# Kernel optimization log

Hardware: AMD Instinct MI355X
Metric: run time of the kernel (lower is better)

## Reference

```python
import jax, jax.numpy as jnp
import numpy as np

B, T, D = 2, 2048, 2048
H = 8
DK = 256   # head_qk_dim
DV = 512   # head_v_dim
C = 64     # retention chunk size
EPS = 1e-5
ROPE_BASE = 10000.0


def _rotary(x):
    # x: [B, T, H, DK], non-interleaved (rotate-half) rotary over full head dim
    half = DK // 2
    inv_freq = 1.0 / (ROPE_BASE ** (jnp.arange(0, DK, 2, dtype=jnp.float32) / DK))
    freqs = jnp.arange(T, dtype=jnp.float32)[:, None] * inv_freq[None, :]  # [T, half]
    cos = jnp.cos(freqs)[None, :, None, :].astype(x.dtype)
    sin = jnp.sin(freqs)[None, :, None, :].astype(x.dtype)
    x1, x2 = x[..., :half], x[..., half:]
    return jnp.concatenate([x1 * cos - x2 * sin, x2 * cos + x1 * sin], axis=-1)


def setup_inputs() -> dict:
    key = jax.random.key(0)
    ks = jax.random.split(key, 6)
    s = 2.0 ** (-2.5) * (2.0 / 2048.0) ** 0.5  # xavier_uniform-ish scale, gain 2^-2.5
    return {
        "hidden_states": jax.random.normal(ks[0], (B, T, D), jnp.float32),
        "Wq": jax.random.normal(ks[1], (H * DK, D), jnp.float32) * s,
        "Wk": jax.random.normal(ks[2], (H * DK, D), jnp.float32) * s,
        "Wv": jax.random.normal(ks[3], (H * DV, D), jnp.float32) * s,
        "Wg": jax.random.normal(ks[4], (H * DV, D), jnp.float32) * s,
        "Wo": jax.random.normal(ks[5], (D, H * DV), jnp.float32) * s,
        "g_norm_weight": jnp.ones((DV,), jnp.float32),
    }


def reference(hidden_states, Wq, Wk, Wv, Wg, Wo, g_norm_weight):
    x = hidden_states  # [B, T, D]
    q = (x @ Wq.T).reshape(B, T, H, DK)
    k = (x @ Wk.T).reshape(B, T, H, DK)
    q = _rotary(q)
    k = _rotary(k)
    q = q.transpose(0, 2, 1, 3) * (DK ** -0.5)        # [B, H, T, DK]
    k = k.transpose(0, 2, 1, 3)                       # [B, H, T, DK]
    v = (x @ Wv.T).reshape(B, T, H, DV).transpose(0, 2, 1, 3)  # [B, H, T, DV]

    # RetNet multi-scale per-head decay
    logb = jnp.log(1.0 - 2.0 ** (-5.0 - jnp.arange(H, dtype=jnp.float32)))  # [H]
    i = jnp.arange(C, dtype=jnp.float32)
    # intra-chunk decay mask b^{i-j} for i>=j: [H, C, C]
    Dmask = jnp.where(i[:, None] >= i[None, :],
                      jnp.exp(logb[:, None, None] * (i[:, None] - i[None, :])), 0.0)
    q_dec = jnp.exp(logb[:, None] * (i + 1.0))        # [H, C]  decay applied to q vs carried state
    k_dec = jnp.exp(logb[:, None] * (C - 1.0 - i))    # [H, C]  decay applied to k for state update
    chunk_dec = jnp.exp(logb * C)                     # [H]

    N = T // C
    qc = q.reshape(B, H, N, C, DK).transpose(2, 0, 1, 3, 4)  # [N, B, H, C, DK]
    kc = k.reshape(B, H, N, C, DK).transpose(2, 0, 1, 3, 4)
    vc = v.reshape(B, H, N, C, DV).transpose(2, 0, 1, 3, 4)

    def body(S, inp):
        qi, ki, vi = inp  # [B,H,C,DK], [B,H,C,DK], [B,H,C,DV]
        inter = jnp.einsum('bhcd,bhdv->bhcv', qi * q_dec[None, :, :, None], S)
        scores = jnp.einsum('bhcd,bhmd->bhcm', qi, ki) * Dmask[None]
        o = inter + jnp.einsum('bhcm,bhmv->bhcv', scores, vi)
        S_new = S * chunk_dec[None, :, None, None] + \
                jnp.einsum('bhcd,bhcv->bhdv', ki * k_dec[None, :, :, None], vi)
        return S_new, o

    S0 = jnp.zeros((B, H, DK, DV), x.dtype)
    _, oc = jax.lax.scan(body, S0, (qc, kc, vc))  # oc: [N, B, H, C, DV]
    o = oc.transpose(1, 2, 0, 3, 4).reshape(B, H, T, DV).transpose(0, 2, 1, 3)  # [B, T, H, DV]

    g = (x @ Wg.T).reshape(B, T, H, DV)
    # fused RMSNorm + swish gate (per head_v_dim)
    o_n = o * jax.lax.rsqrt(jnp.mean(o * o, axis=-1, keepdims=True) + EPS) * g_norm_weight
    o = o_n * (g * jax.nn.sigmoid(g))
    return o.reshape(B, T, H * DV) @ Wo.T  # [B, T, D]
```

## Files before the change

kernel.cpp:

```cpp
#include <hip/hip_runtime.h>


typedef unsigned short u16;
typedef unsigned int u32;
typedef short bf16x8 __attribute__((ext_vector_type(8)));
typedef short s16x4 __attribute__((ext_vector_type(4)));
typedef float f32x4 __attribute__((ext_vector_type(4)));
typedef u32 u32x2 __attribute__((ext_vector_type(2)));

typedef __attribute__((address_space(3))) u32 lds_u32;
typedef __attribute__((address_space(1))) const u32 gbl_u32;

__device__ __forceinline__ float bf2f(u16 u) {
    union { u32 i; float f; } x; x.i = ((u32)u) << 16; return x.f;
}
__device__ __forceinline__ u16 f2bf(float f) {
    union { float f; u32 i; } x; x.f = f;
    u32 u = x.i;
    u += 0x7fffu + ((u >> 16) & 1u);
    return (u16)(u >> 16);
}
__device__ __forceinline__ f32x4 mfma16(bf16x8 a, bf16x8 b, f32x4 c) {
    return __builtin_amdgcn_mfma_f32_16x16x32_bf16(a, b, c, 0, 0, 0);
}
__device__ __forceinline__ void gload16(const u16* g, u16* lds) {
    __builtin_amdgcn_global_load_lds((gbl_u32*)(unsigned long long)g,
                                     (lds_u32*)(u32)(unsigned long long)lds, 16, 0, 0);
}

__global__ __launch_bounds__(256)
void cvt_bf16(const float* __restrict__ src, u16* __restrict__ dst)
{
    size_t i = ((size_t)blockIdx.x * 256 + threadIdx.x) * 8;
    f32x4 a = *(const f32x4*)(src + i);
    f32x4 b = *(const f32x4*)(src + i + 4);
    bf16x8 r;
#pragma unroll
    for (int j = 0; j < 4; j++) { r[j] = (short)f2bf(a[j]); r[j + 4] = (short)f2bf(b[j]); }
    *(bf16x8*)(dst + i) = r;
}

__global__ __launch_bounds__(512, 2)
void gemm256(const u16* __restrict__ A, const u16* __restrict__ Bm,
             u16* __restrict__ C, int N, int K)
{
    __shared__ __align__(16) u16 As[2][2][256 * 32];
    __shared__ __align__(16) u16 Bs[2][2][256 * 32];
    const int tid = threadIdx.x;
    const int lane = tid & 63, wave = tid >> 6;
    const int quad = lane >> 4, l16 = lane & 15;
    const int wm = wave >> 2, wn = wave & 3;
    const int tn = blockIdx.x, tm = blockIdx.y;
    const int NTm1 = K / 64 - 1;
    const u16* Abase = A + (size_t)tm * 256 * K;
    const u16* Bbase = Bm + (size_t)tn * 256 * K;
    const int gr = tid >> 2;
    const int gc = (tid & 3) * 8;
    const int wv64 = wave * 64;

    f32x4 acc[8][4];
#pragma unroll
    for (int i = 0; i < 8; i++)
#pragma unroll
        for (int j = 0; j < 4; j++) acc[i][j] = (f32x4){0.f, 0.f, 0.f, 0.f};

    bf16x8 bq[8];
    bf16x8 af[4];

#define STAGE(arr, bf, kc, Gb, kt) do {                                         \
    int kt_ = (kt); kt_ = (kt_ > NTm1) ? NTm1 : kt_;                            \
    const u16* s_ = (Gb) + (size_t)gr * K + (size_t)kt_ * 64 + (kc) * 32 + gc;  \
    gload16(s_,                 &arr[bf][kc][wv64 * 8]);                        \
    gload16(s_ + (size_t)128 * K, &arr[bf][kc][(512 + wv64) * 8]);              \
} while (0)

#define LDA(bf, kc, mg) do {                                                    \
    _Pragma("unroll")                                                           \
    for (int j = 0; j < 4; j++)                                                 \
        af[j] = *(const bf16x8*)&As[bf][kc][(wm * 128 + (mg) * 64 + j * 16 + l16) * 32 + quad * 8]; \
} while (0)

#define LDB(bf) do {                                                            \
    _Pragma("unroll")                                                           \
    for (int kc_ = 0; kc_ < 2; kc_++)                                           \
        _Pragma("unroll")                                                       \
        for (int n_ = 0; n_ < 4; n_++)                                          \
            bq[kc_ * 4 + n_] = *(const bf16x8*)&Bs[bf][kc_][(wn * 64 + n_ * 16 + l16) * 32 + quad * 8]; \
} while (0)

#define MM16(kc, mg) do {                                                       \
    _Pragma("unroll")                                                           \
    for (int j = 0; j < 4; j++)                                                 \
        _Pragma("unroll")                                                       \
        for (int n_ = 0; n_ < 4; n_++)                                          \
            acc[(mg) * 4 + j][n_] = mfma16(af[j], bq[(kc) * 4 + n_], acc[(mg) * 4 + j][n_]); \
} while (0)

#define BAR   __builtin_amdgcn_s_barrier()
#define LGKM0 asm volatile("s_waitcnt lgkmcnt(0)" ::: "memory")
#define VM6   asm volatile("s_waitcnt vmcnt(6)" ::: "memory")
#define PRIO1 __builtin_amdgcn_s_setprio(1)
#define PRIO0 __builtin_amdgcn_s_setprio(0)

    STAGE(Bs, 0, 0, Bbase, 0);
    STAGE(Bs, 0, 1, Bbase, 0);
    STAGE(As, 0, 0, Abase, 0);
    STAGE(As, 0, 1, Abase, 0);
    asm volatile("s_waitcnt vmcnt(4)" ::: "memory");
    STAGE(Bs, 1, 0, Bbase, 1);
    STAGE(Bs, 1, 1, Bbase, 1);
    STAGE(As, 1, 0, Abase, 1);
    asm volatile("s_waitcnt vmcnt(6)" ::: "memory");
    BAR;

    const int NI = K / 128;
    for (int it = 0; it < NI; ++it) {
        const int t0 = 2 * it;
        LDB(0); LDA(0, 0, 0); STAGE(As, 1, 1, Abase, t0 + 1);
        BAR; LGKM0; PRIO1; MM16(0, 0); PRIO0; BAR;
        LDA(0, 0, 1); STAGE(Bs, 0, 0, Bbase, t0 + 2);
        BAR; LGKM0; PRIO1; MM16(0, 1); PRIO0; BAR;
        LDA(0, 1, 0); STAGE(Bs, 0, 1, Bbase, t0 + 2);
        BAR; LGKM0; PRIO1; MM16(1, 0); PRIO0; BAR;
        LDA(0, 1, 1); STAGE(As, 0, 0, Abase, t0 + 2);
        BAR; LGKM0; PRIO1; MM16(1, 1); PRIO0; VM6; BAR;
        LDB(1); LDA(1, 0, 0); STAGE(As, 0, 1, Abase, t0 + 2);
        BAR; LGKM0; PRIO1; MM16(0, 0); PRIO0; BAR;
        LDA(1, 0, 1); STAGE(Bs, 1, 0, Bbase, t0 + 3);
        BAR; LGKM0; PRIO1; MM16(0, 1); PRIO0; BAR;
        LDA(1, 1, 0); STAGE(Bs, 1, 1, Bbase, t0 + 3);
        BAR; LGKM0; PRIO1; MM16(1, 0); PRIO0; BAR;
        LDA(1, 1, 1); STAGE(As, 1, 0, Abase, t0 + 3);
        BAR; LGKM0; PRIO1; MM16(1, 1); PRIO0; VM6; BAR;
    }
    asm volatile("s_waitcnt vmcnt(0)" ::: "memory");

    const int row0 = tm * 256 + wm * 128 + quad * 4;
    const int col0 = tn * 256 + wn * 64 + l16;
#pragma unroll
    for (int mt = 0; mt < 8; mt++)
#pragma unroll
        for (int nt = 0; nt < 4; nt++)
#pragma unroll
            for (int r = 0; r < 4; r++)
                C[(size_t)(row0 + mt * 16 + r) * N + col0 + nt * 16] = f2bf(acc[mt][nt][r]);

#undef STAGE
#undef LDA
#undef LDB
#undef MM16
}

__global__ __launch_bounds__(512, 2)
void gemm256v(const u16* __restrict__ A, const u16* __restrict__ Bm,
              float* __restrict__ C, int N, int K)
{
    __shared__ __align__(16) u16 As[2][2][256 * 32];
    __shared__ __align__(16) u16 Bs[2][2][128 * 32];
    const int tid = threadIdx.x;
    const int lane = tid & 63, wave = tid >> 6;
    const int quad = lane >> 4, l16 = lane & 15;
    const int wm = wave >> 2, wn = wave & 3;
    const int tn = blockIdx.x, tm = blockIdx.y;
    const int NTm1 = K / 64 - 1;
    const u16* Abase = A + (size_t)tm * 256 * K;
    const u16* Bbase = Bm + (size_t)tn * 128 * K;
    const int gr = tid >> 2;
    const int gc = (tid & 3) * 8;
    const int wv64 = wave * 64;

    f32x4 acc[8][2];
#pragma unroll
    for (int i = 0; i < 8; i++)
#pragma unroll
        for (int j = 0; j < 2; j++) acc[i][j] = (f32x4){0.f, 0.f, 0.f, 0.f};

    bf16x8 bq[4];
    bf16x8 af[4];

#define STAGEA(bf, kc, kt) do {                                                 \
    int kt_ = (kt); kt_ = (kt_ > NTm1) ? NTm1 : kt_;                            \
    const u16* s_ = Abase + (size_t)gr * K + (size_t)kt_ * 64 + (kc) * 32 + gc; \
    gload16(s_,                   &As[bf][kc][wv64 * 8]);                       \
    gload16(s_ + (size_t)128 * K, &As[bf][kc][(512 + wv64) * 8]);               \
} while (0)

#define STAGEB(bf, kc, kt) do {                                                 \
    int kt_ = (kt); kt_ = (kt_ > NTm1) ? NTm1 : kt_;                            \
    const u16* s_ = Bbase + (size_t)gr * K + (size_t)kt_ * 64 + (kc) * 32 + gc; \
    gload16(s_, &Bs[bf][kc][wv64 * 8]);                                         \
} while (0)

#define LDAv(bf, kc, mg) do {                                                   \
    _Pragma("unroll")                                                           \
    for (int j = 0; j < 4; j++)                                                 \
        af[j] = *(const bf16x8*)&As[bf][kc][(wm * 128 + (mg) * 64 + j * 16 + l16) * 32 + quad * 8]; \
} while (0)

#define LDBv(bf) do {                                                           \
    _Pragma("unroll")                                                           \
    for (int kc_ = 0; kc_ < 2; kc_++)                                           \
        _Pragma("unroll")                                                       \
        for (int n_ = 0; n_ < 2; n_++)                                          \
            bq[kc_ * 2 + n_] = *(const bf16x8*)&Bs[bf][kc_][(wn * 32 + n_ * 16 + l16) * 32 + quad * 8]; \
} while (0)

#define MM8(kc, mg) do {                                                        \
    _Pragma("unroll")                                                           \
    for (int j = 0; j < 4; j++)                                                 \
        _Pragma("unroll")                                                       \
        for (int n_ = 0; n_ < 2; n_++)                                          \
            acc[(mg) * 4 + j][n_] = mfma16(af[j], bq[(kc) * 2 + n_], acc[(mg) * 4 + j][n_]); \
} while (0)

#define VM4 asm volatile("s_waitcnt vmcnt(4)" ::: "memory")

    STAGEB(0, 0, 0); STAGEB(0, 1, 0); STAGEA(0, 0, 0); STAGEA(0, 1, 0);
    STAGEB(1, 0, 1); STAGEB(1, 1, 1); STAGEA(1, 0, 1);
    VM4;
    BAR;

    const int NI = K / 128;
    for (int it = 0; it < NI; ++it) {
        const int t0 = 2 * it;
        LDBv(0); LDAv(0, 0, 0); STAGEA(1, 1, t0 + 1);
        BAR; LGKM0; PRIO1; MM8(0, 0); PRIO0; BAR;
        LDAv(0, 0, 1); STAGEB(0, 0, t0 + 2);
        BAR; LGKM0; PRIO1; MM8(0, 1); PRIO0; BAR;
        LDAv(0, 1, 0); STAGEB(0, 1, t0 + 2);
        BAR; LGKM0; PRIO1; MM8(1, 0); PRIO0; BAR;
        LDAv(0, 1, 1); STAGEA(0, 0, t0 + 2);
        BAR; LGKM0; PRIO1; MM8(1, 1); PRIO0; VM4; BAR;
        LDBv(1); LDAv(1, 0, 0); STAGEA(0, 1, t0 + 2);
        BAR; LGKM0; PRIO1; MM8(0, 0); PRIO0; BAR;
        LDAv(1, 0, 1); STAGEB(1, 0, t0 + 3);
        BAR; LGKM0; PRIO1; MM8(0, 1); PRIO0; BAR;
        LDAv(1, 1, 0); STAGEB(1, 1, t0 + 3);
        BAR; LGKM0; PRIO1; MM8(1, 0); PRIO0; BAR;
        LDAv(1, 1, 1); STAGEA(1, 0, t0 + 3);
        BAR; LGKM0; PRIO1; MM8(1, 1); PRIO0; VM4; BAR;
    }
    asm volatile("s_waitcnt vmcnt(0)" ::: "memory");

    const int row0 = tm * 256 + wm * 128 + quad * 4;
    const int col0 = tn * 128 + wn * 32 + l16;
#pragma unroll
    for (int mt = 0; mt < 8; mt++)
#pragma unroll
        for (int nt = 0; nt < 2; nt++)
#pragma unroll
            for (int r = 0; r < 4; r++)
                C[(size_t)(row0 + mt * 16 + r) * N + col0 + nt * 16] = acc[mt][nt][r];

#undef STAGEA
#undef STAGEB
#undef LDAv
#undef LDBv
#undef MM8
#undef VM4
#undef BAR
#undef LGKM0
#undef VM6
#undef PRIO1
#undef PRIO0
}

__global__ __launch_bounds__(256, 2)
void rotary_scores(u16* __restrict__ q, const u16* __restrict__ k,
                   u16* __restrict__ kT, u16* __restrict__ P)
{
    __shared__ u16 qS[64 * 264];
    __shared__ u16 kS[64 * 264];
    const int tid = threadIdx.x;
    const int lane = tid & 63, wave = tid >> 6;
    const int quad = lane >> 4, l16 = lane & 15;
    const int bx = blockIdx.x;
    const int bh = bx & 15, n = bx >> 4;
    const int b = bh >> 3, h = bh & 7;
    const int t0 = n * 64;

    const int row = tid >> 2;
    const int j0 = (tid & 3) * 32;
    const size_t rowbase = (size_t)(b * 2048 + t0 + row) * 4096 + h * 256;
    const float tpos = (float)(t0 + row);
#pragma unroll
    for (int i = 0; i < 4; i++) {
        int j = j0 + i * 8;
        bf16x8 x1 = *(const bf16x8*)(q + rowbase + j);
        bf16x8 x2 = *(const bf16x8*)(q + rowbase + j + 128);
        bf16x8 y1 = *(const bf16x8*)(k + rowbase + j);
        bf16x8 y2 = *(const bf16x8*)(k + rowbase + j + 128);
        bf16x8 o1, o2, p1, p2;
#pragma unroll
        for (int e = 0; e < 8; e++) {
            float inv = expf((-9.210340371976184f / 128.f) * (float)(j + e));
            float ang = tpos * inv;
            float sv = sinf(ang), cv = cosf(ang);
            float a = bf2f((u16)x1[e]), bb = bf2f((u16)x2[e]);
            o1[e] = (short)f2bf((a * cv - bb * sv) * 0.0625f);
            o2[e] = (short)f2bf((bb * cv + a * sv) * 0.0625f);
            float e1 = bf2f((u16)y1[e]), e2 = bf2f((u16)y2[e]);
            p1[e] = (short)f2bf(e1 * cv - e2 * sv);
            p2[e] = (short)f2bf(e2 * cv + e1 * sv);
        }
        *(bf16x8*)(q + rowbase + j)       = o1;
        *(bf16x8*)(q + rowbase + j + 128) = o2;
        *(bf16x8*)(qS + row * 264 + j)       = o1;
        *(bf16x8*)(qS + row * 264 + j + 128) = o2;
        *(bf16x8*)(kS + row * 264 + j)       = p1;
        *(bf16x8*)(kS + row * 264 + j + 128) = p2;
    }
    __syncthreads();

    const float logb = logf(1.0f - exp2f(-5.0f - (float)h));
    f32x4 sc[4];
#pragma unroll
    for (int i = 0; i < 4; i++) sc[i] = (f32x4){0.f, 0.f, 0.f, 0.f};
#pragma unroll
    for (int kc = 0; kc < 8; kc++) {
        bf16x8 af = *(const bf16x8*)(qS + (wave * 16 + l16) * 264 + kc * 32 + quad * 8);
#pragma unroll
        for (int mt = 0; mt < 4; mt++) {
            bf16x8 bk = *(const bf16x8*)(kS + (mt * 16 + l16) * 264 + kc * 32 + quad * 8);
            sc[mt] = mfma16(af, bk, sc[mt]);
        }
    }
    u16* Pb = P + ((size_t)(bh * 32 + n)) * 64 * 64;
#pragma unroll
    for (int r = 0; r < 4; r++) {
        int cr = wave * 16 + quad * 4 + r;
        float rowe = __expf(logb * (float)(cr - 63));
#pragma unroll
        for (int mt = 0; mt < 4; mt++) {
            int m = mt * 16 + l16;
            float val = (cr >= m) ? sc[mt][r] * rowe : 0.0f;
            Pb[cr * 64 + m] = f2bf(val);
        }
    }

    const int d = tid;
    u16* dst = kT + ((size_t)(bh * 256 + d)) * 2048 + t0;
#pragma unroll
    for (int g8 = 0; g8 < 8; g8++) {
        bf16x8 w;
#pragma unroll
        for (int e = 0; e < 8; e++) w[e] = (short)kS[(g8 * 8 + e) * 264 + d];
        *(bf16x8*)(dst + g8 * 8) = w;
    }
}

__global__ __launch_bounds__(256, 2)
void retention(const u16* __restrict__ Q, const u16* __restrict__ KT,
               const u16* __restrict__ V, const u16* __restrict__ P,
               u16* __restrict__ O)
{
    __shared__ __align__(16) u16 Stf[2][4096];
    __shared__ __align__(16) u16 vsf[2][1024];

    const int tid = threadIdx.x;
    const int lane = tid & 63, wave = tid >> 6;
    const int quad = lane >> 4, l16 = lane & 15;
    const int bx = blockIdx.x;
    const int bh = bx & 15, vt = bx >> 4;
    const int b = bh >> 3, h = bh & 7;

    const float logb = logf(1.0f - exp2f(-5.0f - (float)h));
    const float cdec = __expf(logb * 64.0f);
    float qdecr[4];
#pragma unroll
    for (int r = 0; r < 4; r++)
        qdecr[r] = __expf(logb * (float)(wave * 16 + quad * 4 + r + 1));
    const int w4 = wave * 4;
    const float kdv = __expf(logb * (float)(63 - lane));
    const int vwb = (((lane >> 5) * 4 + ((lane >> 3) & 3)) * 16 + w4) * 8 + (lane & 7);

    for (int i = tid; i < 4096; i += 256) { Stf[0][i] = 0; Stf[1][i] = 0; }

    const u16* Qp  = Q  + (size_t)(b * 2048 + wave * 16 + l16) * 4096 + h * 256 + quad * 8;
    const u16* KTp = KT + (size_t)(bh * 256 + wave * 64 + l16) * 2048 + quad * 8;
    const u16* Pp  = P  + ((size_t)(bh * 32) * 64 + wave * 16 + l16) * 64 + quad * 8;
    const u16* Vp  = V  + (size_t)(b * 2048 + lane) * 4096 + h * 512 + vt * 16 + w4;
    u16* Ob = O + (size_t)(b * 2048 + wave * 16 + quad * 4) * 4096 + h * 512 + vt * 16 + l16;

    f32x4 Sacc[4];
#pragma unroll
    for (int dt = 0; dt < 4; dt++) Sacc[dt] = (f32x4){0.f, 0.f, 0.f, 0.f};

    bf16x8 qfA[8], qfB[8], ktA[8], ktB[8], pfA[2], pfB[2];
    u32x2 vvA, vvB;

#define LOADSET(nn, qf, kt, pf, vvn, nv) do {                                   \
    const int nL = (nn), vL = (nv);                                             \
    _Pragma("unroll")                                                           \
    for (int kc = 0; kc < 8; kc++)                                              \
        qf[kc] = *(const bf16x8*)(Qp + (size_t)nL * (64 * 4096) + kc * 32);     \
    _Pragma("unroll")                                                           \
    for (int dt = 0; dt < 4; dt++)                                              \
        _Pragma("unroll")                                                       \
        for (int kc2 = 0; kc2 < 2; kc2++)                                       \
            kt[dt * 2 + kc2] = *(const bf16x8*)(KTp + dt * (16 * 2048)          \
                                  + (size_t)nL * 64 + kc2 * 32);                \
    _Pragma("unroll")                                                           \
    for (int kc2 = 0; kc2 < 2; kc2++)                                           \
        pf[kc2] = *(const bf16x8*)(Pp + (size_t)nL * (64 * 64) + kc2 * 32);     \
    vvn = *(const u32x2*)(Vp + (size_t)vL * (64 * 4096));                       \
} while (0)

#define STAGEVS(buf, vvC) do {                                                  \
    u16* vd = &vsf[buf][0];                                                     \
    u16 e0 = (u16)(vvC[0] & 0xffff), e1 = (u16)(vvC[0] >> 16);                  \
    u16 e2 = (u16)(vvC[1] & 0xffff), e3 = (u16)(vvC[1] >> 16);                  \
    vd[vwb + 0 * 8] = f2bf(bf2f(e0) * kdv);                                     \
    vd[vwb + 1 * 8] = f2bf(bf2f(e1) * kdv);                                     \
    vd[vwb + 2 * 8] = f2bf(bf2f(e2) * kdv);                                     \
    vd[vwb + 3 * 8] = f2bf(bf2f(e3) * kdv);                                     \
} while (0)

    u32x2 vv0 = *(const u32x2*)(Vp);
    LOADSET(0, qfA, ktA, pfA, vvA, 1);
    STAGEVS(0, vv0);

#define CHUNK(nn, qfC, ktC, pfC, vvC, qfN, ktN, pfN, vvN) do {                  \
    const int nC = (nn);                                                        \
    const int nP = (nC + 1 < 32) ? nC + 1 : 31;                                 \
    const int nV = (nC + 2 < 32) ? nC + 2 : 31;                                 \
    LOADSET(nP, qfN, ktN, pfN, vvN, nV);                   \
    asm volatile("s_waitcnt lgkmcnt(0)" ::: "memory");                          \
    __builtin_amdgcn_s_barrier();                                               \
    __builtin_amdgcn_sched_barrier(0);                                          \
    STAGEVS((nC + 1) & 1, vvC);                                    \
                       \
    f32x4 oacc = (f32x4){0.f, 0.f, 0.f, 0.f};                                   \
    _Pragma("unroll")                                                           \
    for (int kc = 0; kc < 8; kc++) {                                            \
        bf16x8 bs = *(const bf16x8*)&Stf[(nC + 1) & 1][(kc * 4 + quad) * 128 + l16 * 8]; \
        oacc = mfma16(qfC[kc], bs, oacc);                                       \
    }                                                                           \
                                        \
    bf16x8 bv0 = *(const bf16x8*)&vsf[nC & 1][(0 * 4 + quad) * 128 + l16 * 8];  \
    bf16x8 bv1 = *(const bf16x8*)&vsf[nC & 1][(1 * 4 + quad) * 128 + l16 * 8];  \
                                      \
    _Pragma("unroll")                                                           \
    for (int dt = 0; dt < 4; dt++)                                              \
        _Pragma("unroll")                                                       \
        for (int e = 0; e < 4; e++) Sacc[dt][e] *= cdec;                        \
    _Pragma("unroll")                                                           \
    for (int dt = 0; dt < 4; dt++) {                                            \
        Sacc[dt] = mfma16(ktC[dt * 2 + 0], bv0, Sacc[dt]);                      \
        Sacc[dt] = mfma16(ktC[dt * 2 + 1], bv1, Sacc[dt]);                      \
    }                                                                           \
                                              \
    _Pragma("unroll")                                                           \
    for (int r = 0; r < 4; r++) oacc[r] *= qdecr[r];                            \
    oacc = mfma16(pfC[0], bv0, oacc);                                           \
    oacc = mfma16(pfC[1], bv1, oacc);                                           \
    _Pragma("unroll")                                                           \
    for (int r = 0; r < 4; r++)                                                 \
        Ob[(size_t)(nC * 64 + r) * 4096] = f2bf(oacc[r]);                       \
                               \
    _Pragma("unroll")                                                           \
    for (int dt = 0; dt < 4; dt++) {                                            \
        s16x4 w;                                                                \
        _Pragma("unroll")                                                       \
        for (int r = 0; r < 4; r++) w[r] = (short)f2bf(Sacc[dt][r]);            \
        const int kct = 2 * wave + (dt >> 1);                                   \
        const int qt  = (2 * dt + (quad >> 1)) & 3;                             \
        *(s16x4*)&Stf[nC & 1][(kct * 4 + qt) * 128 + l16 * 8 + 4 * (quad & 1)] = w; \
    }                                                                           \
} while (0)

    for (int m = 0; m < 16; m++) {
        CHUNK(2 * m,     qfA, ktA, pfA, vvA, qfB, ktB, pfB, vvB);
        CHUNK(2 * m + 1, qfB, ktB, pfB, vvB, qfA, ktA, pfA, vvA);
    }
#undef CHUNK
#undef STAGEVS
#undef LOADSET
}

__global__ __launch_bounds__(256)
void norm_gate(const u16* __restrict__ O, const u16* __restrict__ G,
               const float* __restrict__ gw, u16* __restrict__ ON)
{
    const int lane = threadIdx.x & 63;
    const size_t row = (size_t)blockIdx.x * 4 + (threadIdx.x >> 6);
    bf16x8 ov = *(const bf16x8*)(O + row * 512 + lane * 8);
    bf16x8 gv = *(const bf16x8*)(G + row * 512 + lane * 8);
    f32x4 w0 = *(const f32x4*)(gw + lane * 8);
    f32x4 w1 = *(const f32x4*)(gw + lane * 8 + 4);
    float of[8], gf[8];
    float ss = 0.f;
#pragma unroll
    for (int j = 0; j < 8; j++) {
        of[j] = bf2f((u16)ov[j]);
        gf[j] = bf2f((u16)gv[j]);
        ss += of[j] * of[j];
    }
#pragma unroll
    for (int off = 32; off > 0; off >>= 1) ss += __shfl_down(ss, off);
    ss = __shfl(ss, 0);
    const float rms = rsqrtf(ss * (1.0f / 512.0f) + 1e-5f);
    bf16x8 res;
#pragma unroll
    for (int j = 0; j < 8; j++) {
        float wj = (j < 4) ? w0[j] : w1[j - 4];
        float xn = of[j] * rms * wj;
        float sg = gf[j] / (1.f + __expf(-gf[j]));
        res[j] = (short)f2bf(xn * sg);
    }
    *(bf16x8*)(ON + row * 512 + lane * 8) = res;
}

extern "C" void kernel_launch(void* const* d_in, const int* in_sizes, int n_in,
                              void* d_out, int out_size, void* d_ws, size_t ws_size,
                              hipStream_t stream)
{
    const float* x  = (const float*)d_in[0];
    const float* Wq = (const float*)d_in[1];
    const float* Wk = (const float*)d_in[2];
    const float* Wv = (const float*)d_in[3];
    const float* Wg = (const float*)d_in[4];
    const float* Wo = (const float*)d_in[5];
    const float* gw = (const float*)d_in[6];
    float* out = (float*)d_out;

    const size_t M8 = (size_t)4096 * 2048;
    u16* Pb = (u16*)d_ws;
    u16* qk = Pb + (size_t)16 * 32 * 64 * 64;
    u16* kT = qk + 2 * M8;
    u16* v  = kT + M8;
    u16* o  = v + 2 * M8;
    u16* xb = o + 2 * M8;
    u16* g  = qk;
    u16* on = v;
    u16* wt = kT;

    dim3 blk(256, 1, 1), blk512(512, 1, 1);
    cvt_bf16<<<dim3(4096, 1, 1), blk, 0, stream>>>(x, xb);

    cvt_bf16<<<dim3(2048, 1, 1), blk, 0, stream>>>(Wq, wt);
    cvt_bf16<<<dim3(2048, 1, 1), blk, 0, stream>>>(Wk, wt + (size_t)2048 * 2048);
    gemm256<<<dim3(16, 16, 1), blk512, 0, stream>>>(xb, wt, qk, 4096, 2048);
    cvt_bf16<<<dim3(4096, 1, 1), blk, 0, stream>>>(Wv, wt);
    gemm256<<<dim3(16, 16, 1), blk512, 0, stream>>>(xb, wt, v, 4096, 2048);

    rotary_scores<<<dim3(512, 1, 1), blk, 0, stream>>>(qk, qk + 2048, kT, Pb);
    retention<<<dim3(512, 1, 1), blk, 0, stream>>>(qk, kT, v, Pb, o);

    cvt_bf16<<<dim3(4096, 1, 1), blk, 0, stream>>>(Wg, kT);
    gemm256<<<dim3(16, 16, 1), blk512, 0, stream>>>(xb, kT, g, 4096, 2048);
    norm_gate<<<dim3(8192, 1, 1), blk, 0, stream>>>(o, g, gw, on);
    cvt_bf16<<<dim3(4096, 1, 1), blk, 0, stream>>>(Wo, kT);
    gemm256v<<<dim3(16, 16, 1), blk512, 0, stream>>>(on, kT, out, 2048, 4096);
}
```

Before: 621.5 us.

## Precompute RoPE table and widen retention blocks to 32 value columns

Adds a kernel that precomputes a cos/sin table per position and frequency, so rotary_scores loads these values instead of evaluating expf/sinf/cosf per element. The retention kernel moves to 512-thread blocks, each covering 32 value columns with half as many blocks. Waves are split into chunk-row groups and value halves, and the LDS layouts of state and V are padded and transposed. This roughly halves the redundant Q/KT/P loads across blocks, at the cost of fewer blocks in flight (256 on the GPU) and extra global traffic for the table.

```diff
diff --git a/kernel.cpp b/kernel.cpp
--- a/kernel.cpp
+++ b/kernel.cpp
@@ -38,6 +38,17 @@
 #pragma unroll
     for (int j = 0; j < 4; j++) { r[j] = (short)f2bf(a[j]); r[j + 4] = (short)f2bf(b[j]); }
     *(bf16x8*)(dst + i) = r;
+}
+
+__global__ __launch_bounds__(256)
+void rope_table(float* __restrict__ tab)
+{
+    int idx = blockIdx.x * 256 + threadIdx.x;
+    int t = idx >> 7, jp = idx & 127;
+    float inv = expf((-9.210340371976184f / 128.f) * (float)jp);
+    float ang = (float)t * inv;
+    tab[idx * 2 + 0] = cosf(ang);
+    tab[idx * 2 + 1] = sinf(ang);
 }
 
 __global__ __launch_bounds__(512, 2)
@@ -267,7 +278,8 @@
 
 __global__ __launch_bounds__(256, 2)
 void rotary_scores(u16* __restrict__ q, const u16* __restrict__ k,
-                   u16* __restrict__ kT, u16* __restrict__ P)
+                   u16* __restrict__ kT, u16* __restrict__ P,
+                   const float* __restrict__ tab)
 {
     __shared__ u16 qS[64 * 264];
     __shared__ u16 kS[64 * 264];
@@ -282,7 +294,7 @@
     const int row = tid >> 2;
     const int j0 = (tid & 3) * 32;
     const size_t rowbase = (size_t)(b * 2048 + t0 + row) * 4096 + h * 256;
-    const float tpos = (float)(t0 + row);
+    const float* tb = tab + (size_t)(t0 + row) * 256;
 #pragma unroll
     for (int i = 0; i < 4; i++) {
         int j = j0 + i * 8;
@@ -290,12 +302,16 @@
         bf16x8 x2 = *(const bf16x8*)(q + rowbase + j + 128);
         bf16x8 y1 = *(const bf16x8*)(k + rowbase + j);
         bf16x8 y2 = *(const bf16x8*)(k + rowbase + j + 128);
+        f32x4 tv0 = *(const f32x4*)(tb + 2 * j);
+        f32x4 tv1 = *(const f32x4*)(tb + 2 * j + 4);
+        f32x4 tv2 = *(const f32x4*)(tb + 2 * j + 8);
+        f32x4 tv3 = *(const f32x4*)(tb + 2 * j + 12);
+        float cv_[8] = {tv0[0], tv0[2], tv1[0], tv1[2], tv2[0], tv2[2], tv3[0], tv3[2]};
+        float sv_[8] = {tv0[1], tv0[3], tv1[1], tv1[3], tv2[1], tv2[3], tv3[1], tv3[3]};
         bf16x8 o1, o2, p1, p2;
 #pragma unroll
         for (int e = 0; e < 8; e++) {
-            float inv = expf((-9.210340371976184f / 128.f) * (float)(j + e));
-            float ang = tpos * inv;
-            float sv = sinf(ang), cv = cosf(ang);
+            float cv = cv_[e], sv = sv_[e];
             float a = bf2f((u16)x1[e]), bb = bf2f((u16)x2[e]);
             o1[e] = (short)f2bf((a * cv - bb * sv) * 0.0625f);
             o2[e] = (short)f2bf((bb * cv + a * sv) * 0.0625f);
@@ -349,13 +365,13 @@
     }
 }
 
-__global__ __launch_bounds__(256, 2)
+__global__ __launch_bounds__(512, 1)
 void retention(const u16* __restrict__ Q, const u16* __restrict__ KT,
                const u16* __restrict__ V, const u16* __restrict__ P,
                u16* __restrict__ O)
 {
-    __shared__ __align__(16) u16 Stf[2][4096];
-    __shared__ __align__(16) u16 vsf[2][1024];
+    __shared__ u16 St[2][32 * 264];
+    __shared__ u16 vsT[2][32 * 72];
 
     const int tid = threadIdx.x;
     const int lane = tid & 63, wave = tid >> 6;
@@ -363,30 +379,36 @@
     const int bx = blockIdx.x;
     const int bh = bx & 15, vt = bx >> 4;
     const int b = bh >> 3, h = bh & 7;
+    const int cgrp = wave >> 1, vhalf = wave & 1;
 
     const float logb = logf(1.0f - exp2f(-5.0f - (float)h));
     const float cdec = __expf(logb * 64.0f);
+
+    int cr[4];
     float qdecr[4];
 #pragma unroll
-    for (int r = 0; r < 4; r++)
-        qdecr[r] = __expf(logb * (float)(wave * 16 + quad * 4 + r + 1));
-    const int w4 = wave * 4;
-    const float kdv = __expf(logb * (float)(63 - lane));
-    const int vwb = (((lane >> 5) * 4 + ((lane >> 3) & 3)) * 16 + w4) * 8 + (lane & 7);
-
-    for (int i = tid; i < 4096; i += 256) { Stf[0][i] = 0; Stf[1][i] = 0; }
-
-    const u16* Qp  = Q  + (size_t)(b * 2048 + wave * 16 + l16) * 4096 + h * 256 + quad * 8;
-    const u16* KTp = KT + (size_t)(bh * 256 + wave * 64 + l16) * 2048 + quad * 8;
-    const u16* Pp  = P  + ((size_t)(bh * 32) * 64 + wave * 16 + l16) * 64 + quad * 8;
-    const u16* Vp  = V  + (size_t)(b * 2048 + lane) * 4096 + h * 512 + vt * 16 + w4;
-    u16* Ob = O + (size_t)(b * 2048 + wave * 16 + quad * 4) * 4096 + h * 512 + vt * 16 + l16;
-
-    f32x4 Sacc[4];
-#pragma unroll
-    for (int dt = 0; dt < 4; dt++) Sacc[dt] = (f32x4){0.f, 0.f, 0.f, 0.f};
-
-    bf16x8 qfA[8], qfB[8], ktA[8], ktB[8], pfA[2], pfB[2];
+    for (int r = 0; r < 4; r++) {
+        cr[r] = cgrp * 16 + quad * 4 + r;
+        qdecr[r] = __expf(logb * (float)(cr[r] + 1));
+    }
+    const int mv = tid >> 3;
+    const int vc4 = (tid & 7) * 4;
+    const float kdv = __expf(logb * (float)(63 - mv));
+
+    for (int i = tid; i < 32 * 264; i += 512) { St[0][i] = 0; St[1][i] = 0; }
+
+    const u16* Qp  = Q  + (size_t)(b * 2048 + cgrp * 16 + l16) * 4096 + h * 256 + quad * 8;
+    const u16* KTp = KT + (size_t)(bh * 256 + wave * 32 + l16) * 2048 + quad * 8;
+    const u16* Pp  = P  + ((size_t)(bh * 32) * 64 + cgrp * 16 + l16) * 64 + quad * 8;
+    const u16* Vp  = V  + (size_t)(b * 2048 + mv) * 4096 + h * 512 + vt * 32 + vc4;
+
+    f32x4 Sacc[2][2];
+#pragma unroll
+    for (int dt = 0; dt < 2; dt++)
+#pragma unroll
+        for (int nt = 0; nt < 2; nt++) Sacc[dt][nt] = (f32x4){0.f, 0.f, 0.f, 0.f};
+
+    bf16x8 qfA[8], qfB[8], ktA[4], ktB[4], pfA[2], pfB[2];
     u32x2 vvA, vvB;
 
 #define LOADSET(nn, qf, kt, pf, vvn, nv) do {                                   \
@@ -395,78 +417,93 @@
     for (int kc = 0; kc < 8; kc++)                                              \
         qf[kc] = *(const bf16x8*)(Qp + (size_t)nL * (64 * 4096) + kc * 32);     \
     _Pragma("unroll")                                                           \
-    for (int dt = 0; dt < 4; dt++)                                              \
+    for (int dt = 0; dt < 2; dt++)                                              \
         _Pragma("unroll")                                                       \
         for (int kc2 = 0; kc2 < 2; kc2++)                                       \
-            kt[dt * 2 + kc2] = *(const bf16x8*)(KTp + dt * (16 * 2048)          \
-                                  + (size_t)nL * 64 + kc2 * 32);                \
+            kt[dt * 2 + kc2] = *(const bf16x8*)(KTp + dt * (16 * 2048) + nL * 64 + kc2 * 32); \
     _Pragma("unroll")                                                           \
     for (int kc2 = 0; kc2 < 2; kc2++)                                           \
         pf[kc2] = *(const bf16x8*)(Pp + (size_t)nL * (64 * 64) + kc2 * 32);     \
     vvn = *(const u32x2*)(Vp + (size_t)vL * (64 * 4096));                       \
 } while (0)
 
-#define STAGEVS(buf, vvC) do {                                                  \
-    u16* vd = &vsf[buf][0];                                                     \
-    u16 e0 = (u16)(vvC[0] & 0xffff), e1 = (u16)(vvC[0] >> 16);                  \
-    u16 e2 = (u16)(vvC[1] & 0xffff), e3 = (u16)(vvC[1] >> 16);                  \
-    vd[vwb + 0 * 8] = f2bf(bf2f(e0) * kdv);                                     \
-    vd[vwb + 1 * 8] = f2bf(bf2f(e1) * kdv);                                     \
-    vd[vwb + 2 * 8] = f2bf(bf2f(e2) * kdv);                                     \
-    vd[vwb + 3 * 8] = f2bf(bf2f(e3) * kdv);                                     \
-} while (0)
-
     u32x2 vv0 = *(const u32x2*)(Vp);
     LOADSET(0, qfA, ktA, pfA, vvA, 1);
-    STAGEVS(0, vv0);
+    {
+        u16 e0 = (u16)(vv0[0] & 0xffff), e1 = (u16)(vv0[0] >> 16);
+        u16 e2 = (u16)(vv0[1] & 0xffff), e3 = (u16)(vv0[1] >> 16);
+        vsT[0][(vc4 + 0) * 72 + mv] = f2bf(bf2f(e0) * kdv);
+        vsT[0][(vc4 + 1) * 72 + mv] = f2bf(bf2f(e1) * kdv);
+        vsT[0][(vc4 + 2) * 72 + mv] = f2bf(bf2f(e2) * kdv);
+        vsT[0][(vc4 + 3) * 72 + mv] = f2bf(bf2f(e3) * kdv);
+    }
 
 #define CHUNK(nn, qfC, ktC, pfC, vvC, qfN, ktN, pfN, vvN) do {                  \
     const int nC = (nn);                                                        \
     const int nP = (nC + 1 < 32) ? nC + 1 : 31;                                 \
     const int nV = (nC + 2 < 32) ? nC + 2 : 31;                                 \
-    LOADSET(nP, qfN, ktN, pfN, vvN, nV);                   \
+    LOADSET(nP, qfN, ktN, pfN, vvN, nV);         \
     asm volatile("s_waitcnt lgkmcnt(0)" ::: "memory");                          \
     __builtin_amdgcn_s_barrier();                                               \
     __builtin_amdgcn_sched_barrier(0);                                          \
-    STAGEVS((nC + 1) & 1, vvC);                                    \
-                       \
+    {                                 \
+        u16* vd = &vsT[(nC + 1) & 1][0];                                        \
+        u16 e0 = (u16)(vvC[0] & 0xffff), e1 = (u16)(vvC[0] >> 16);              \
+        u16 e2 = (u16)(vvC[1] & 0xffff), e3 = (u16)(vvC[1] >> 16);              \
+        vd[(vc4 + 0) * 72 + mv] = f2bf(bf2f(e0) * kdv);                         \
+        vd[(vc4 + 1) * 72 + mv] = f2bf(bf2f(e1) * kdv);                         \
+        vd[(vc4 + 2) * 72 + mv] = f2bf(bf2f(e2) * kdv);                         \
+        vd[(vc4 + 3) * 72 + mv] = f2bf(bf2f(e3) * kdv);                         \
+    }                                                                           \
+                        \
     f32x4 oacc = (f32x4){0.f, 0.f, 0.f, 0.f};                                   \
     _Pragma("unroll")                                                           \
     for (int kc = 0; kc < 8; kc++) {                                            \
-        bf16x8 bs = *(const bf16x8*)&Stf[(nC + 1) & 1][(kc * 4 + quad) * 128 + l16 * 8]; \
+        bf16x8 bs = *(const bf16x8*)(&St[(nC + 1) & 1][0]                       \
+                     + (vhalf * 16 + l16) * 264 + kc * 32 + quad * 8);          \
         oacc = mfma16(qfC[kc], bs, oacc);                                       \
     }                                                                           \
-                                        \
-    bf16x8 bv0 = *(const bf16x8*)&vsf[nC & 1][(0 * 4 + quad) * 128 + l16 * 8];  \
-    bf16x8 bv1 = *(const bf16x8*)&vsf[nC & 1][(1 * 4 + quad) * 128 + l16 * 8];  \
-                                      \
-    _Pragma("unroll")                                                           \
-    for (int dt = 0; dt < 4; dt++)                                              \
-        _Pragma("unroll")                                                       \
-        for (int e = 0; e < 4; e++) Sacc[dt][e] *= cdec;                        \
-    _Pragma("unroll")                                                           \
-    for (int dt = 0; dt < 4; dt++) {                                            \
-        Sacc[dt] = mfma16(ktC[dt * 2 + 0], bv0, Sacc[dt]);                      \
-        Sacc[dt] = mfma16(ktC[dt * 2 + 1], bv1, Sacc[dt]);                      \
+                        \
+    _Pragma("unroll")                                                           \
+    for (int dt = 0; dt < 2; dt++)                                              \
+        _Pragma("unroll")                                                       \
+        for (int nt = 0; nt < 2; nt++)                                          \
+            _Pragma("unroll")                                                   \
+            for (int e = 0; e < 4; e++) Sacc[dt][nt][e] *= cdec;                \
+    _Pragma("unroll")                                                           \
+    for (int kc2 = 0; kc2 < 2; kc2++) {                                         \
+        bf16x8 bv0 = *(const bf16x8*)(&vsT[nC & 1][0] + l16 * 72 + kc2 * 32 + quad * 8);        \
+        bf16x8 bv1 = *(const bf16x8*)(&vsT[nC & 1][0] + (16 + l16) * 72 + kc2 * 32 + quad * 8); \
+        _Pragma("unroll")                                                       \
+        for (int dt = 0; dt < 2; dt++) {                                        \
+            Sacc[dt][0] = mfma16(ktC[dt * 2 + kc2], bv0, Sacc[dt][0]);          \
+            Sacc[dt][1] = mfma16(ktC[dt * 2 + kc2], bv1, Sacc[dt][1]);          \
+        }                                                                       \
     }                                                                           \
                                               \
     _Pragma("unroll")                                                           \
     for (int r = 0; r < 4; r++) oacc[r] *= qdecr[r];                            \
-    oacc = mfma16(pfC[0], bv0, oacc);                                           \
-    oacc = mfma16(pfC[1], bv1, oacc);                                           \
+    _Pragma("unroll")                                                           \
+    for (int kc2 = 0; kc2 < 2; kc2++) {                                         \
+        bf16x8 bv = *(const bf16x8*)(&vsT[nC & 1][0]                            \
+                     + (vhalf * 16 + l16) * 72 + kc2 * 32 + quad * 8);          \
+        oacc = mfma16(pfC[kc2], bv, oacc);                                      \
+    }                                                                           \
     _Pragma("unroll")                                                           \
     for (int r = 0; r < 4; r++)                                                 \
-        Ob[(size_t)(nC * 64 + r) * 4096] = f2bf(oacc[r]);                       \
-                               \
-    _Pragma("unroll")                                                           \
-    for (int dt = 0; dt < 4; dt++) {                                            \
-        s16x4 w;                                                                \
-        _Pragma("unroll")                                                       \
-        for (int r = 0; r < 4; r++) w[r] = (short)f2bf(Sacc[dt][r]);            \
-        const int kct = 2 * wave + (dt >> 1);                                   \
-        const int qt  = (2 * dt + (quad >> 1)) & 3;                             \
-        *(s16x4*)&Stf[nC & 1][(kct * 4 + qt) * 128 + l16 * 8 + 4 * (quad & 1)] = w; \
-    }                                                                           \
+        O[(size_t)(b * 2048 + nC * 64 + cr[r]) * 4096 + h * 512 + vt * 32       \
+          + vhalf * 16 + l16] = f2bf(oacc[r]);                                  \
+                                       \
+    _Pragma("unroll")                                                           \
+    for (int dt = 0; dt < 2; dt++)                                              \
+        _Pragma("unroll")                                                       \
+        for (int nt = 0; nt < 2; nt++) {                                        \
+            s16x4 w;                                                            \
+            _Pragma("unroll")                                                   \
+            for (int r = 0; r < 4; r++) w[r] = (short)f2bf(Sacc[dt][nt][r]);    \
+            *(s16x4*)(&St[nC & 1][0] + (nt * 16 + l16) * 264 + wave * 32        \
+                      + dt * 16 + quad * 4) = w;                                \
+        }                                                                       \
 } while (0)
 
     for (int m = 0; m < 16; m++) {
@@ -474,7 +511,6 @@
         CHUNK(2 * m + 1, qfB, ktB, pfB, vvB, qfA, ktA, pfA, vvA);
     }
 #undef CHUNK
-#undef STAGEVS
 #undef LOADSET
 }
 
@@ -531,11 +567,13 @@
     u16* v  = kT + M8;
     u16* o  = v + 2 * M8;
     u16* xb = o + 2 * M8;
+    float* tab = (float*)(xb + M8);
     u16* g  = qk;
     u16* on = v;
     u16* wt = kT;
 
     dim3 blk(256, 1, 1), blk512(512, 1, 1);
+    rope_table<<<dim3(1024, 1, 1), blk, 0, stream>>>(tab);
     cvt_bf16<<<dim3(4096, 1, 1), blk, 0, stream>>>(x, xb);
 
     cvt_bf16<<<dim3(2048, 1, 1), blk, 0, stream>>>(Wq, wt);
@@ -544,8 +582,8 @@
     cvt_bf16<<<dim3(4096, 1, 1), blk, 0, stream>>>(Wv, wt);
     gemm256<<<dim3(16, 16, 1), blk512, 0, stream>>>(xb, wt, v, 4096, 2048);
 
-    rotary_scores<<<dim3(512, 1, 1), blk, 0, stream>>>(qk, qk + 2048, kT, Pb);
-    retention<<<dim3(512, 1, 1), blk, 0, stream>>>(qk, kT, v, Pb, o);
+    rotary_scores<<<dim3(512, 1, 1), blk, 0, stream>>>(qk, qk + 2048, kT, Pb, tab);
+    retention<<<dim3(256, 1, 1), blk512, 0, stream>>>(qk, kT, v, Pb, o);
 
     cvt_bf16<<<dim3(4096, 1, 1), blk, 0, stream>>>(Wg, kT);
     gemm256<<<dim3(16, 16, 1), blk512, 0, stream>>>(xb, kT, g, 4096, 2048);
```

Result: faster. 593.9 us (-4.4%).
